# Kernel tuning notes

Measured on AMD Instinct MI355X. Metric: run time of the kernel, lower is better.

## Reference

```python
import jax, jax.numpy as jnp
import numpy as np

NUM_HEADS = 16
ROPE_BASE = 10000.0


def _rope_cos_sin(T, head_dim, dtype):
    # standard rotary: angles[t, i] = t * base^(-2i/head_dim), half-split layout
    inv_freq = 1.0 / (ROPE_BASE ** (jnp.arange(0, head_dim, 2, dtype=jnp.float32) / head_dim))
    ang = jnp.arange(T, dtype=jnp.float32)[:, None] * inv_freq[None, :]  # [T, hd/2]
    cos = jnp.concatenate([jnp.cos(ang), jnp.cos(ang)], axis=-1).astype(dtype)  # [T, hd]
    sin = jnp.concatenate([jnp.sin(ang), jnp.sin(ang)], axis=-1).astype(dtype)
    return cos, sin


def _rotate_half(t):
    t1, t2 = jnp.split(t, 2, axis=-1)
    return jnp.concatenate([-t2, t1], axis=-1)


def _apply_rope(t, cos, sin):
    # t: [B, H, T, hd]; cos/sin: [T, hd]
    return t * cos[None, None] + _rotate_half(t) * sin[None, None]


def setup_inputs() -> dict:
    key = jax.random.key(0)
    B, T, C = 2, 2048, 1024
    k1, k2, k3 = jax.random.split(key, 3)
    x = jax.random.normal(k1, (B, T, C), dtype=jnp.float32)
    w_attn = jax.random.normal(k2, (C, 3 * C), dtype=jnp.float32) * (C ** -0.5)
    w_proj = jax.random.normal(k3, (C, C), dtype=jnp.float32) * (C ** -0.5)
    return {"x": x, "w_attn": w_attn, "w_proj": w_proj}


def reference(x, w_attn, w_proj):
    B, T, C = x.shape
    H = NUM_HEADS
    hd = C // H

    qkv = x @ w_attn  # [B, T, 3C]
    q, k, v = jnp.split(qkv, 3, axis=-1)
    # [B, T, C] -> [B, H, T, hd]
    q = q.reshape(B, T, H, hd).transpose(0, 2, 1, 3)
    k = k.reshape(B, T, H, hd).transpose(0, 2, 1, 3)
    v = v.reshape(B, T, H, hd).transpose(0, 2, 1, 3)

    cos, sin = _rope_cos_sin(T, hd, x.dtype)
    q = _apply_rope(q, cos, sin)
    k = _apply_rope(k, cos, sin)

    scale = 1.0 / np.sqrt(hd).astype(np.float32)
    att = jnp.einsum('bhqd,bhkd->bhqk', q, k) * scale  # [B, H, T, T]
    causal = jnp.tril(jnp.ones((T, T), dtype=bool))
    att = jnp.where(causal[None, None], att, jnp.array(-jnp.inf, dtype=att.dtype))
    att = jax.nn.softmax(att, axis=-1)
    y = jnp.einsum('bhqk,bhkd->bhqd', att, v)  # [B, H, T, hd]
    y = y.transpose(0, 2, 1, 3).reshape(B, T, C)
    return y @ w_proj
```

## Files before the change

### kernel.cpp

```cpp
#include <hip/hip_runtime.h>

typedef unsigned short u16;
typedef unsigned int u32;
typedef unsigned long long u64;
typedef __attribute__((ext_vector_type(8))) short s16x8;
typedef __attribute__((ext_vector_type(8))) __bf16 bf16x8;
typedef __attribute__((ext_vector_type(4))) float fx4;
typedef __attribute__((ext_vector_type(16))) float fx16;
typedef __attribute__((ext_vector_type(2))) u32 u32x2;
typedef __attribute__((ext_vector_type(4))) u32 u32x4;

__device__ __forceinline__ fx4 mfma_16x16x32(s16x8 a, s16x8 b, fx4 c) {
  return __builtin_amdgcn_mfma_f32_16x16x32_bf16(
      __builtin_bit_cast(bf16x8, a), __builtin_bit_cast(bf16x8, b), c, 0, 0, 0);
}
__device__ __forceinline__ fx16 mfma_32x32x16(s16x8 a, s16x8 b, fx16 c) {
  return __builtin_amdgcn_mfma_f32_32x32x16_bf16(
      __builtin_bit_cast(bf16x8, a), __builtin_bit_cast(bf16x8, b), c, 0, 0, 0);
}

__device__ __forceinline__ u16 f2bf(float f) {
  u32 u = __builtin_bit_cast(u32, f);
  u32 r = u + 0x7fffu + ((u >> 16) & 1u);
  return (u16)(r >> 16);
}
__device__ __forceinline__ float bf2f(u16 h) {
  u32 u = ((u32)h) << 16;
  return __builtin_bit_cast(float, u);
}

__device__ __forceinline__ u32 cvtpk(float lo, float hi) {
  u32 r;
  asm("v_cvt_pk_bf16_f32 %0, %1, %2" : "=v"(r) : "v"(lo), "v"(hi));
  return r;
}

__device__ __forceinline__ float max3f(float a, float b, float c) {
  float r;
  asm("v_max3_f32 %0, %1, %2, %3" : "=v"(r) : "v"(a), "v"(b), "v"(c));
  return r;
}

__device__ __forceinline__ void plswap(u32& x, u32& y) {
  typedef __attribute__((ext_vector_type(2))) unsigned int uix2;
  uix2 r = __builtin_amdgcn_permlane32_swap(x, y, false, false);
  x = r[0];
  y = r[1];
}

__device__ __forceinline__ float xhalf_max(float v) {
  u32 a = __builtin_bit_cast(u32, v), b = a;
  plswap(a, b);
  return fmaxf(__builtin_bit_cast(float, a), __builtin_bit_cast(float, b));
}
__device__ __forceinline__ float xhalf_sum(float v) {
  u32 a = __builtin_bit_cast(u32, v), b = a;
  plswap(a, b);
  return __builtin_bit_cast(float, a) + __builtin_bit_cast(float, b);
}

__device__ __forceinline__ void gload16(const void* g, void* l) {
  __builtin_amdgcn_global_load_lds(
      (const __attribute__((address_space(1))) u32*)g,
      (__attribute__((address_space(3))) u32*)l, 16, 0, 0);
}

#define B_ 2
#define T_ 2048
#define C_ 1024
#define H_ 16
#define HD_ 64
#define BH_ 32
#define M_ 4096
#define CF_ 0.18033688011112042f

__global__ __launch_bounds__(256) void prep_k(
    const float* __restrict__ x, const float* __restrict__ wa,
    const float* __restrict__ wp, u16* __restrict__ xb, u16* __restrict__ waT,
    u16* __restrict__ wpT, float* __restrict__ ct, float* __restrict__ st) {
  __shared__ u16 T_s[64 * 72];
  int b = blockIdx.x, tid = threadIdx.x;
  if (b < 2048) {
    int id = b * 256 + tid;
    const fx4* p = (const fx4*)(x + (u64)id * 8);
    fx4 v0 = p[0], v1 = p[1];
    s16x8 r;
#pragma unroll
    for (int j = 0; j < 4; ++j) {
      r[j] = (short)f2bf(v0[j]);
      r[4 + j] = (short)f2bf(v1[j]);
    }
    *((s16x8*)xb + id) = r;
  } else if (b < 3072) {
    const float* W;
    u16* WT;
    int Ncols, bx, by;
    if (b < 2816) {
      int i = b - 2048;
      W = wa; WT = waT; Ncols = 3072; bx = i % 48; by = i / 48;
    } else {
      int i = b - 2816;
      W = wp; WT = wpT; Ncols = 1024; bx = i % 16; by = i / 16;
    }
    int c0 = bx * 64, r0 = by * 64;
#pragma unroll
    for (int it = 0; it < 4; ++it) {
      int idx = it * 256 + tid;
      int r = idx >> 4, c4 = (idx & 15) * 4;
      fx4 v = *(const fx4*)(W + (u64)(r0 + r) * Ncols + c0 + c4);
#pragma unroll
      for (int j = 0; j < 4; ++j) T_s[(c4 + j) * 72 + r] = f2bf(v[j]);
    }
    __syncthreads();
#pragma unroll
    for (int it = 0; it < 2; ++it) {
      int idx = it * 256 + tid;
      int rc = idx >> 3, c8 = (idx & 7) * 8;
      s16x8 v = *(const s16x8*)(T_s + rc * 72 + c8);
      *(s16x8*)(WT + (u64)(c0 + rc) * 1024 + r0 + c8) = v;
    }
  } else {
    int id = (b - 3072) * 256 + tid;
    int t = id >> 5, i = id & 31;
    float f = exp2f(-(float)i * (13.287712379549449f / 32.0f));
    float a = (float)t * f;
    float s, c;
    sincosf(a, &s, &c);
    ct[id] = c;
    st[id] = s;
  }
}

__global__ __launch_bounds__(256, 3) void gemm1_k(
    const u16* __restrict__ A, const u16* __restrict__ B,
    u16* __restrict__ Qo, u16* __restrict__ Ko, u16* __restrict__ Vo,
    const float* __restrict__ ct, const float* __restrict__ st,
    int M, int N, int K) {
  __shared__ u16 AsS[3][128 * 32];
  __shared__ u16 BsS[3][128 * 32];
  int tid = threadIdx.x, lane = tid & 63, w = tid >> 6;
  int wm = w >> 1, wn = w & 1, l15 = lane & 15, l4 = lane >> 4;
  int nwg = gridDim.x * gridDim.y;
  int id = blockIdx.y * gridDim.x + blockIdx.x;
  int qq = nwg >> 3;
  id = (id & 7) * qq + (id >> 3);
  int m0 = (id / gridDim.x) * 128, n0 = (id % gridDim.x) * 128;
  fx4 acc[4][4] = {};

  const u16* asrc[2];
  const u16* bsrc[2];
#pragma unroll
  for (int g = 0; g < 2; ++g) {
    int idx = g * 256 + tid;
    int row = idx >> 2, slot = (idx & 3) ^ (row & 3);
    asrc[g] = A + (u64)(m0 + row) * K + slot * 8;
    bsrc[g] = B + (u64)(n0 + row) * K + slot * 8;
  }

#define GSTAGE(S, KOFF)                                                      \
  do {                                                                       \
    _Pragma("unroll")                                                        \
    for (int g_ = 0; g_ < 2; ++g_) {                                         \
      gload16(asrc[g_] + (KOFF), (char*)AsS[S] + g_ * 4096 + tid * 16);      \
      gload16(bsrc[g_] + (KOFF), (char*)BsS[S] + g_ * 4096 + tid * 16);      \
    }                                                                        \
  } while (0)

#define GCOMP(S)                                                             \
  do {                                                                       \
    s16x8 a_[4], b_[4];                                                      \
    _Pragma("unroll")                                                        \
    for (int mi_ = 0; mi_ < 4; ++mi_) {                                      \
      int r_ = wm * 64 + mi_ * 16 + l15;                                     \
      a_[mi_] = *(const s16x8*)((const char*)AsS[S] + r_ * 64 +              \
                                ((l4 ^ (r_ & 3)) * 16));                     \
    }                                                                        \
    _Pragma("unroll")                                                        \
    for (int ni_ = 0; ni_ < 4; ++ni_) {                                      \
      int r_ = wn * 64 + ni_ * 16 + l15;                                     \
      b_[ni_] = *(const s16x8*)((const char*)BsS[S] + r_ * 64 +              \
                                ((l4 ^ (r_ & 3)) * 16));                     \
    }                                                                        \
    _Pragma("unroll")                                                        \
    for (int mi_ = 0; mi_ < 4; ++mi_)                                        \
      _Pragma("unroll")                                                      \
      for (int ni_ = 0; ni_ < 4; ++ni_)                                      \
        acc[mi_][ni_] = mfma_16x16x32(a_[mi_], b_[ni_], acc[mi_][ni_]);      \
  } while (0)

  int NT = K >> 5;
  GSTAGE(0, 0);
  GSTAGE(1, 32);
  int s0 = 0, s1 = 1, s2 = 2;
  for (int t = 0; t < NT; ++t) {
    __builtin_amdgcn_s_barrier();
    __builtin_amdgcn_sched_barrier(0);
    if (t + 2 < NT) GSTAGE(s2, (t + 2) * 32);
    __builtin_amdgcn_sched_barrier(0);
    if (t < NT - 2)
      asm volatile("s_waitcnt vmcnt(8)" ::: "memory");
    else if (t == NT - 2)
      asm volatile("s_waitcnt vmcnt(4)" ::: "memory");
    else
      asm volatile("s_waitcnt vmcnt(0)" ::: "memory");
    __builtin_amdgcn_s_barrier();
    __builtin_amdgcn_sched_barrier(0);
    GCOMP(s0);
    int tmp = s0;
    s0 = s1;
    s1 = s2;
    s2 = tmp;
  }
#undef GSTAGE
#undef GCOMP

#pragma unroll
  for (int mi = 0; mi < 4; ++mi)
#pragma unroll
    for (int r = 0; r < 4; ++r) {
      int row = m0 + wm * 64 + mi * 16 + l4 * 4 + r;
      int b2 = row >> 11, t = row & (T_ - 1);
#pragma unroll
      for (int ni = 0; ni < 2; ++ni) {
        int col = n0 + wn * 64 + ni * 16 + l15;
        int qi = col >> 10, h = (col >> 6) & 15, d = ni * 16 + l15;
        float lo = acc[mi][ni][r], hi = acc[mi][ni + 2][r];
        if (qi == 2) {
          u64 vbase =
              ((((u64)(b2 * H_ + h)) * (T_ / 8) + (t >> 3)) * HD_ + d) * 8 + (t & 7);
          Vo[vbase] = f2bf(lo);
          Vo[vbase + 32 * 8] = f2bf(hi);
        } else {
          float c = ct[t * 32 + d], s = st[t * 32 + d];
          float sc = (qi == 0) ? CF_ : 1.0f;
          u16* dst = (qi == 0) ? Qo : Ko;
          u64 base = ((((u64)(b2 * H_ + h)) * 8 + (d >> 3)) * T_ + t) * 8 + (d & 7);
          dst[base] = f2bf((lo * c - hi * s) * sc);
          dst[base + (u64)4 * T_ * 8] = f2bf((hi * c + lo * s) * sc);
        }
      }
    }
}

__global__ __launch_bounds__(256, 2) void gemm2_nb(
    const u16* __restrict__ A, const u16* __restrict__ B, float* __restrict__ C,
    int M, int N, int K) {
  __shared__ u16 lds[4][2][2][64 * 32];
  int tid = threadIdx.x, lane = tid & 63, w = tid >> 6;
  int wm = w >> 1, wn = w & 1, l15 = lane & 15, l4 = lane >> 4;
  int nwg = gridDim.x * gridDim.y;
  int id = blockIdx.y * gridDim.x + blockIdx.x;
  int qq = nwg >> 3;
  id = (id & 7) * qq + (id >> 3);
  int m0 = (id / gridDim.x) * 128 + wm * 64;
  int n0 = (id % gridDim.x) * 128 + wn * 64;
  fx4 acc[4][4] = {};

  const u16* asrc[4];
  const u16* bsrc[4];
  int doff[4];
#pragma unroll
  for (int g = 0; g < 4; ++g) {
    int p = g * 64 + lane;
    int row = p >> 2, slot = (p & 3) ^ (row & 3);
    doff[g] = p * 16;
    asrc[g] = A + (u64)(m0 + row) * K + slot * 8;
    bsrc[g] = B + (u64)(n0 + row) * K + slot * 8;
  }

#define STG(BUF, KOFF)                                                       \
  do {                                                                       \
    _Pragma("unroll")                                                        \
    for (int g_ = 0; g_ < 4; ++g_) {                                         \
      gload16(asrc[g_] + (KOFF), (char*)lds[w][BUF][0] + doff[g_]);          \
      gload16(bsrc[g_] + (KOFF), (char*)lds[w][BUF][1] + doff[g_]);          \
    }                                                                        \
  } while (0)

#define CMP(BUF)                                                             \
  do {                                                                       \
    s16x8 a_[4], b_[4];                                                      \
    _Pragma("unroll")                                                        \
    for (int mi_ = 0; mi_ < 4; ++mi_) {                                      \
      int r_ = mi_ * 16 + l15;                                               \
      a_[mi_] = *(const s16x8*)((const char*)lds[w][BUF][0] + r_ * 64 +      \
                                ((l4 ^ (r_ & 3)) * 16));                     \
    }                                                                        \
    _Pragma("unroll")                                                        \
    for (int ni_ = 0; ni_ < 4; ++ni_) {                                      \
      int r_ = ni_ * 16 + l15;                                               \
      b_[ni_] = *(const s16x8*)((const char*)lds[w][BUF][1] + r_ * 64 +      \
                                ((l4 ^ (r_ & 3)) * 16));                     \
    }                                                                        \
    _Pragma("unroll")                                                        \
    for (int mi_ = 0; mi_ < 4; ++mi_)                                        \
      _Pragma("unroll")                                                      \
      for (int ni_ = 0; ni_ < 4; ++ni_)                                      \
        acc[mi_][ni_] = mfma_16x16x32(a_[mi_], b_[ni_], acc[mi_][ni_]);      \
  } while (0)

  int NT = K >> 5;
  STG(0, 0);
  for (int t = 0; t < NT; ++t) {
    __builtin_amdgcn_sched_barrier(0);
    if (t + 1 < NT) {
      STG((t + 1) & 1, (t + 1) * 32);
      asm volatile("s_waitcnt vmcnt(8)" ::: "memory");
    } else {
      asm volatile("s_waitcnt vmcnt(0)" ::: "memory");
    }
    __builtin_amdgcn_sched_barrier(0);
    CMP(t & 1);
  }
#undef STG
#undef CMP

#pragma unroll
  for (int mi = 0; mi < 4; ++mi)
#pragma unroll
    for (int ni = 0; ni < 4; ++ni)
#pragma unroll
      for (int r = 0; r < 4; ++r) {
        u64 row = (u64)(m0 + mi * 16 + l4 * 4 + r);
        int col = n0 + ni * 16 + l15;
        C[row * N + col] = acc[mi][ni][r];
      }
}

#define LOADK(KC, KVI)                                                 \
  do {                                                                 \
    _Pragma("unroll")                                                  \
    for (int ks_ = 0; ks_ < 4; ++ks_)                                  \
      KC[ks_] = *(const s16x8*)(kp[ks_] + (u64)(KVI) * 256);           \
  } while (0)

#define LOADV(VC, KVI)                                                 \
  do {                                                                 \
    const u16* vk_ = vpb + (u64)(KVI) * 2048;                          \
    VC[0] = *(const s16x8*)(vk_);                                      \
    VC[1] = *(const s16x8*)(vk_ + 256);                                \
    VC[2] = *(const s16x8*)(vk_ + 1024);                               \
    VC[3] = *(const s16x8*)(vk_ + 1280);                               \
  } while (0)

#define ATTN_STEP(KC, VC, KVI)                                                \
  do {                                                                        \
    fx16 s_ = {};                                                             \
    __builtin_amdgcn_s_setprio(1);                                            \
    _Pragma("unroll")                                                         \
    for (int ks_ = 0; ks_ < 4; ++ks_)                                         \
      s_ = mfma_32x32x16(KC[ks_], qf[ks_], s_);                               \
    __builtin_amdgcn_s_setprio(0);                                            \
    if ((KVI) == jt) {                                                        \
      _Pragma("unroll")                                                       \
      for (int r_ = 0; r_ < 16; ++r_) {                                       \
        int cr_ = (r_ & 3) + 8 * (r_ >> 2) + 4 * h;                           \
        s_[r_] = (cr_ > ql) ? -1e30f : s_[r_];                                \
      }                                                                       \
    }                                                                         \
    float u0_ = max3f(s_[0], s_[1], s_[2]);                                   \
    float u1_ = max3f(s_[3], s_[4], s_[5]);                                   \
    float u2_ = max3f(s_[6], s_[7], s_[8]);                                   \
    float u3_ = max3f(s_[9], s_[10], s_[11]);                                 \
    float u4_ = max3f(s_[12], s_[13], s_[14]);                                \
    float v0_ = max3f(u0_, u1_, s_[15]);                                      \
    float v1_ = max3f(u2_, u3_, u4_);                                         \
    float rowmax_ = xhalf_max(fmaxf(v0_, v1_));                               \
    if (!__all(rowmax_ <= m + 8.f)) {                                         \
      float mnew_ = fmaxf(m, rowmax_);                                        \
      float corr_ = exp2f(m - mnew_);                                         \
      l *= corr_;                                                             \
      oL *= corr_;                                                            \
      oH *= corr_;                                                            \
      m = mnew_;                                                              \
    }                                                                         \
    float p_[16];                                                             \
    _Pragma("unroll")                                                         \
    for (int r_ = 0; r_ < 16; ++r_) p_[r_] = exp2f(s_[r_] - m);               \
    float a0_ = (p_[0] + p_[8]) + (p_[1] + p_[9]);                            \
    float a1_ = (p_[2] + p_[10]) + (p_[3] + p_[11]);                          \
    float a2_ = (p_[4] + p_[12]) + (p_[5] + p_[13]);                          \
    float a3_ = (p_[6] + p_[14]) + (p_[7] + p_[15]);                          \
    l += xhalf_sum((a0_ + a1_) + (a2_ + a3_));                                \
    u32 x0_ = cvtpk(p_[0], p_[1]), x1_ = cvtpk(p_[2], p_[3]);                 \
    u32 y0_ = cvtpk(p_[4], p_[5]), y1_ = cvtpk(p_[6], p_[7]);                 \
    plswap(x0_, y0_);                                                         \
    plswap(x1_, y1_);                                                         \
    u32x4 f0w_ = {x0_, x1_, y0_, y1_};                                        \
    u32 x2_ = cvtpk(p_[8], p_[9]), x3_ = cvtpk(p_[10], p_[11]);               \
    u32 y2_ = cvtpk(p_[12], p_[13]), y3_ = cvtpk(p_[14], p_[15]);             \
    plswap(x2_, y2_);                                                         \
    plswap(x3_, y3_);                                                         \
    u32x4 f1w_ = {x2_, x3_, y2_, y3_};                                        \
    s16x8 pf0_ = __builtin_bit_cast(s16x8, f0w_);                             \
    s16x8 pf1_ = __builtin_bit_cast(s16x8, f1w_);                             \
    __builtin_amdgcn_s_setprio(1);                                            \
    oL = mfma_32x32x16(VC[0], pf0_, oL);                                      \
    oH = mfma_32x32x16(VC[1], pf0_, oH);                                      \
    oL = mfma_32x32x16(VC[2], pf1_, oL);                                      \
    oH = mfma_32x32x16(VC[3], pf1_, oH);                                      \
    __builtin_amdgcn_s_setprio(0);                                            \
  } while (0)

#define OSTRIDE 68

__global__ __launch_bounds__(256, 3) void attn_fwd_k(
    const u16* __restrict__ Qp, const u16* __restrict__ Kp,
    const u16* __restrict__ Vp, u16* __restrict__ Y) {
  __shared__ float Ob[4 * 32 * OSTRIDE];
  __shared__ float Ml[4 * 32 * 2];
  int tid = threadIdx.x, lane = tid & 63, w = tid >> 6;
  int ql = lane & 31, h = lane >> 5;
  int bh = blockIdx.x & 31;
  int jt = 63 - (blockIdx.x >> 5);
  int q0 = jt * 32;
  int b2 = bh >> 4, head = bh & 15;
  int n = jt + 1;
  int lo = (w * n) >> 2, hi = ((w + 1) * n) >> 2;

  s16x8 qf[4];
#pragma unroll
  for (int ks = 0; ks < 4; ++ks)
    qf[ks] = *(const s16x8*)(Qp + (((u64)bh * 8 + ks * 2 + h) * T_ + q0 + ql) * 8);

  const u16* kp[4];
#pragma unroll
  for (int ks = 0; ks < 4; ++ks)
    kp[ks] = Kp + (((u64)bh * 8 + ks * 2 + h) * T_ + ql) * 8;
  const u16* vpb = Vp + (((u64)bh * (T_ / 8) + h) * HD_ + ql) * 8;

  fx16 oL = {}, oH = {};
  float m = -1e30f, l = 0.f;

  if (lo < hi) {
    s16x8 kA[4], vA[4], kB[4], vB[4];
    LOADK(kA, lo);
    LOADV(vA, lo);
    int kv = lo;
    for (; kv + 1 < hi; kv += 2) {
      LOADK(kB, kv + 1);
      LOADV(vB, kv + 1);
      ATTN_STEP(kA, vA, kv);
      if (kv + 2 < hi) {
        LOADK(kA, kv + 2);
        LOADV(vA, kv + 2);
      }
      ATTN_STEP(kB, vB, kv + 1);
    }
    if (kv < hi) ATTN_STEP(kA, vA, kv);
  }

  {
    float* ob = Ob + (w * 32 + ql) * OSTRIDE;
#pragma unroll
    for (int g = 0; g < 4; ++g) {
      fx4 a = {oL[4 * g], oL[4 * g + 1], oL[4 * g + 2], oL[4 * g + 3]};
      *(fx4*)(ob + 8 * g + 4 * h) = a;
      fx4 b = {oH[4 * g], oH[4 * g + 1], oH[4 * g + 2], oH[4 * g + 3]};
      *(fx4*)(ob + 32 + 8 * g + 4 * h) = b;
    }
    if (h == 0) {
      Ml[(w * 32 + ql) * 2] = m;
      Ml[(w * 32 + ql) * 2 + 1] = l;
    }
  }
  __syncthreads();

  {
    int q = tid >> 3, db = tid & 7;
    float mm0 = Ml[(0 * 32 + q) * 2], ll0 = Ml[(0 * 32 + q) * 2 + 1];
    float mm1 = Ml[(1 * 32 + q) * 2], ll1 = Ml[(1 * 32 + q) * 2 + 1];
    float mm2 = Ml[(2 * 32 + q) * 2], ll2 = Ml[(2 * 32 + q) * 2 + 1];
    float mm3 = Ml[(3 * 32 + q) * 2], ll3 = Ml[(3 * 32 + q) * 2 + 1];
    float mo = fmaxf(fmaxf(mm0, mm1), fmaxf(mm2, mm3));
    float w0 = exp2f(mm0 - mo), w1 = exp2f(mm1 - mo);
    float w2 = exp2f(mm2 - mo), w3 = exp2f(mm3 - mo);
    float rl = 1.0f / (ll0 * w0 + ll1 * w1 + ll2 * w2 + ll3 * w3);
    w0 *= rl; w1 *= rl; w2 *= rl; w3 *= rl;
    const float* ob = Ob + q * OSTRIDE + db * 8;
    fx4 aa = {}, bb = {};
#pragma unroll
    for (int i = 0; i < 4; ++i) {
      float wi = (i == 0) ? w0 : (i == 1) ? w1 : (i == 2) ? w2 : w3;
      fx4 pa = *(const fx4*)(ob + i * 32 * OSTRIDE);
      fx4 pb = *(const fx4*)(ob + i * 32 * OSTRIDE + 4);
      aa += wi * pa;
      bb += wi * pb;
    }
    u32x4 ow;
    ow[0] = cvtpk(aa[0], aa[1]);
    ow[1] = cvtpk(aa[2], aa[3]);
    ow[2] = cvtpk(bb[0], bb[1]);
    ow[3] = cvtpk(bb[2], bb[3]);
    int t = q0 + q;
    *(u32x4*)(Y + ((u64)(b2 * T_ + t)) * C_ + head * HD_ + db * 8) = ow;
  }
}

extern "C" void kernel_launch(void* const* d_in, const int* in_sizes, int n_in,
                              void* d_out, int out_size, void* d_ws, size_t ws_size,
                              hipStream_t stream) {
  (void)in_sizes; (void)n_in; (void)out_size; (void)ws_size;
  const float* x = (const float*)d_in[0];
  const float* w_attn = (const float*)d_in[1];
  const float* w_proj = (const float*)d_in[2];
  float* out = (float*)d_out;

  u16* xb = (u16*)d_ws;
  u16* waT = xb + (u64)M_ * C_;
  u16* wpT = waT + (u64)3 * C_ * C_;
  u16* Qp = wpT + (u64)C_ * C_;
  u16* Kp = Qp + (u64)BH_ * T_ * HD_;
  u16* Vp = Kp + (u64)BH_ * T_ * HD_;
  float* ct = (float*)(Vp + (u64)BH_ * T_ * HD_);
  float* st = ct + T_ * 32;
  u16* yb = xb;

  prep_k<<<3328, 256, 0, stream>>>(x, w_attn, w_proj, xb, waT, wpT, ct, st);

  gemm1_k<<<dim3(24, 32), 256, 0, stream>>>(xb, waT, Qp, Kp, Vp,
                                            ct, st, M_, 3 * C_, C_);

  attn_fwd_k<<<2048, 256, 0, stream>>>(Qp, Kp, Vp, yb);

  gemm2_nb<<<dim3(8, 32), 256, 0, stream>>>(yb, wpT, out, M_, C_, C_);
}
```

Before: 104.8 us.

## Give each wave private LDS tiles in QKV GEMM to drop block barriers

The QKV projection GEMM now has each wave load its own 64-row A and B sub-tiles into a private double-buffered LDS region and wait only on its own vmcnt. This removes both workgroup s_barriers per K step. In exchange, A and B tiles are no longer shared across waves, so global/L2 traffic per block doubles. LDS use grows from 48KB to 64KB and launch bounds drop from 3 to 2 blocks per CU. The pipeline also goes from three stages to two.

```diff
diff --git a/kernel.cpp b/kernel.cpp
--- a/kernel.cpp
+++ b/kernel.cpp
@@ -131,54 +131,56 @@
   }
 }
 
-__global__ __launch_bounds__(256, 3) void gemm1_k(
+__global__ __launch_bounds__(256, 2) void gemm1_nb(
     const u16* __restrict__ A, const u16* __restrict__ B,
     u16* __restrict__ Qo, u16* __restrict__ Ko, u16* __restrict__ Vo,
     const float* __restrict__ ct, const float* __restrict__ st,
     int M, int N, int K) {
-  __shared__ u16 AsS[3][128 * 32];
-  __shared__ u16 BsS[3][128 * 32];
+  __shared__ u16 lds[4][2][2][64 * 32];
   int tid = threadIdx.x, lane = tid & 63, w = tid >> 6;
   int wm = w >> 1, wn = w & 1, l15 = lane & 15, l4 = lane >> 4;
   int nwg = gridDim.x * gridDim.y;
   int id = blockIdx.y * gridDim.x + blockIdx.x;
   int qq = nwg >> 3;
   id = (id & 7) * qq + (id >> 3);
-  int m0 = (id / gridDim.x) * 128, n0 = (id % gridDim.x) * 128;
+  int m0 = (id / gridDim.x) * 128 + wm * 64;
+  int n0 = (id % gridDim.x) * 128 + wn * 64;
   fx4 acc[4][4] = {};
 
-  const u16* asrc[2];
-  const u16* bsrc[2];
-#pragma unroll
-  for (int g = 0; g < 2; ++g) {
-    int idx = g * 256 + tid;
-    int row = idx >> 2, slot = (idx & 3) ^ (row & 3);
+  const u16* asrc[4];
+  const u16* bsrc[4];
+  int doff[4];
+#pragma unroll
+  for (int g = 0; g < 4; ++g) {
+    int p = g * 64 + lane;
+    int row = p >> 2, slot = (p & 3) ^ (row & 3);
+    doff[g] = p * 16;
     asrc[g] = A + (u64)(m0 + row) * K + slot * 8;
     bsrc[g] = B + (u64)(n0 + row) * K + slot * 8;
   }
 
-#define GSTAGE(S, KOFF)                                                      \
+#define STG(BUF, KOFF)                                                       \
   do {                                                                       \
     _Pragma("unroll")                                                        \
-    for (int g_ = 0; g_ < 2; ++g_) {                                         \
-      gload16(asrc[g_] + (KOFF), (char*)AsS[S] + g_ * 4096 + tid * 16);      \
-      gload16(bsrc[g_] + (KOFF), (char*)BsS[S] + g_ * 4096 + tid * 16);      \
+    for (int g_ = 0; g_ < 4; ++g_) {                                         \
+      gload16(asrc[g_] + (KOFF), (char*)lds[w][BUF][0] + doff[g_]);          \
+      gload16(bsrc[g_] + (KOFF), (char*)lds[w][BUF][1] + doff[g_]);          \
     }                                                                        \
   } while (0)
 
-#define GCOMP(S)                                                             \
+#define CMP(BUF)                                                             \
   do {                                                                       \
     s16x8 a_[4], b_[4];                                                      \
     _Pragma("unroll")                                                        \
     for (int mi_ = 0; mi_ < 4; ++mi_) {                                      \
-      int r_ = wm * 64 + mi_ * 16 + l15;                                     \
-      a_[mi_] = *(const s16x8*)((const char*)AsS[S] + r_ * 64 +              \
+      int r_ = mi_ * 16 + l15;                                               \
+      a_[mi_] = *(const s16x8*)((const char*)lds[w][BUF][0] + r_ * 64 +      \
                                 ((l4 ^ (r_ & 3)) * 16));                     \
     }                                                                        \
     _Pragma("unroll")                                                        \
     for (int ni_ = 0; ni_ < 4; ++ni_) {                                      \
-      int r_ = wn * 64 + ni_ * 16 + l15;                                     \
-      b_[ni_] = *(const s16x8*)((const char*)BsS[S] + r_ * 64 +              \
+      int r_ = ni_ * 16 + l15;                                               \
+      b_[ni_] = *(const s16x8*)((const char*)lds[w][BUF][1] + r_ * 64 +      \
                                 ((l4 ^ (r_ & 3)) * 16));                     \
     }                                                                        \
     _Pragma("unroll")                                                        \
@@ -189,40 +191,30 @@
   } while (0)
 
   int NT = K >> 5;
-  GSTAGE(0, 0);
-  GSTAGE(1, 32);
-  int s0 = 0, s1 = 1, s2 = 2;
+  STG(0, 0);
   for (int t = 0; t < NT; ++t) {
-    __builtin_amdgcn_s_barrier();
     __builtin_amdgcn_sched_barrier(0);
-    if (t + 2 < NT) GSTAGE(s2, (t + 2) * 32);
+    if (t + 1 < NT) {
+      STG((t + 1) & 1, (t + 1) * 32);
+      asm volatile("s_waitcnt vmcnt(8)" ::: "memory");
+    } else {
+      asm volatile("s_waitcnt vmcnt(0)" ::: "memory");
+    }
     __builtin_amdgcn_sched_barrier(0);
-    if (t < NT - 2)
-      asm volatile("s_waitcnt vmcnt(8)" ::: "memory");
-    else if (t == NT - 2)
-      asm volatile("s_waitcnt vmcnt(4)" ::: "memory");
-    else
-      asm volatile("s_waitcnt vmcnt(0)" ::: "memory");
-    __builtin_amdgcn_s_barrier();
-    __builtin_amdgcn_sched_barrier(0);
-    GCOMP(s0);
-    int tmp = s0;
-    s0 = s1;
-    s1 = s2;
-    s2 = tmp;
-  }
-#undef GSTAGE
-#undef GCOMP
+    CMP(t & 1);
+  }
+#undef STG
+#undef CMP
 
 #pragma unroll
   for (int mi = 0; mi < 4; ++mi)
 #pragma unroll
     for (int r = 0; r < 4; ++r) {
-      int row = m0 + wm * 64 + mi * 16 + l4 * 4 + r;
+      int row = m0 + mi * 16 + l4 * 4 + r;
       int b2 = row >> 11, t = row & (T_ - 1);
 #pragma unroll
       for (int ni = 0; ni < 2; ++ni) {
-        int col = n0 + wn * 64 + ni * 16 + l15;
+        int col = n0 + ni * 16 + l15;
         int qi = col >> 10, h = (col >> 6) & 15, d = ni * 16 + l15;
         float lo = acc[mi][ni][r], hi = acc[mi][ni + 2][r];
         if (qi == 2) {
@@ -518,8 +510,8 @@
 
   prep_k<<<3328, 256, 0, stream>>>(x, w_attn, w_proj, xb, waT, wpT, ct, st);
 
-  gemm1_k<<<dim3(24, 32), 256, 0, stream>>>(xb, waT, Qp, Kp, Vp,
-                                            ct, st, M_, 3 * C_, C_);
+  gemm1_nb<<<dim3(24, 32), 256, 0, stream>>>(xb, waT, Qp, Kp, Vp,
+                                             ct, st, M_, 3 * C_, C_);
 
   attn_fwd_k<<<2048, 256, 0, stream>>>(Qp, Kp, Vp, yb);
 
```

Measured after the change: 128.5 us. +22.6%, slower.
